# Optimization experiments

Hardware: AMD Instinct MI355X
Metric: run time of the kernel (lower is better)

The kernel has to match this reference:

```python
import jax, jax.numpy as jnp
import numpy as np

INPUT_SIZE = 1024
HIDDEN_SIZE = 1024

def _xavier(key, shape):
    fan_in, fan_out = shape
    limit = np.sqrt(6.0 / (fan_in + fan_out))
    return jax.random.uniform(key, shape, jnp.float32, -limit, limit)

def setup_inputs() -> dict:
    key = jax.random.key(0)
    ks = jax.random.split(key, 9)
    x = jax.random.normal(ks[0], (64, 512, INPUT_SIZE), jnp.float32)
    d = {"x": x}
    names_i = ["W_ii", "W_fi", "W_gi", "W_oi"]
    names_h = ["W_ih", "W_fh", "W_gh", "W_oh"]
    for n, k in zip(names_i, ks[1:5]):
        d[n] = _xavier(k, (INPUT_SIZE, HIDDEN_SIZE))
    for n, k in zip(names_h, ks[5:9]):
        d[n] = _xavier(k, (HIDDEN_SIZE, HIDDEN_SIZE))
    for n in ["b_ii", "b_ih", "b_fi", "b_fh", "b_gi", "b_gh", "b_oi", "b_oh"]:
        d[n] = jnp.zeros((HIDDEN_SIZE,), jnp.float32)
    return d

def _lstm(x, W_ii, W_ih, b_ii, b_ih, W_fi, W_fh, b_fi, b_fh,
          W_gi, W_gh, b_gi, b_gh, W_oi, W_oh, b_oi, b_oh):
    B, S, _ = x.shape
    H = W_ih.shape[0]
    # Fuse the 4 input-side GEMMs into one and hoist out of the recurrence.
    Wi = jnp.concatenate([W_ii, W_fi, W_gi, W_oi], axis=1)          # [I, 4H]
    Wh = jnp.concatenate([W_ih, W_fh, W_gh, W_oh], axis=1)          # [H, 4H]
    bi = jnp.concatenate([b_ii + b_ih, b_fi + b_fh, b_gi + b_gh, b_oi + b_oh])
    xproj = jnp.einsum('bsi,ig->bsg', x, Wi) + bi                    # [B, S, 4H]

    def step(carry, xp_t):
        h, c = carry
        gates = xp_t + h @ Wh                                        # [B, 4H]
        i_t = jax.nn.sigmoid(gates[:, 0 * H:1 * H])
        f_t = jax.nn.sigmoid(gates[:, 1 * H:2 * H])
        g_t = jnp.tanh(gates[:, 2 * H:3 * H])
        o_t = jax.nn.sigmoid(gates[:, 3 * H:4 * H])
        c = f_t * c + i_t * g_t
        h = o_t * jnp.tanh(c)
        return (h, c), None

    h0 = jnp.zeros((B, H), x.dtype)
    c0 = jnp.zeros((B, H), x.dtype)
    (h_t, c_t), _ = jax.lax.scan(step, (h0, c0), jnp.swapaxes(xproj, 0, 1))
    return h_t, c_t

def reference(x, W_ii, W_ih, b_ii, b_ih, W_fi, W_fh, b_fi, b_fh,
              W_gi, W_gh, b_gi, b_gh, W_oi, W_oh, b_oi, b_oh):
    return _lstm(x, W_ii, W_ih, b_ii, b_ih, W_fi, W_fh, b_fi, b_fh,
                 W_gi, W_gh, b_gi, b_gh, W_oi, W_oh, b_oi, b_oh)
```

## Files before the change

### kernel.cpp

```cpp
#include <hip/hip_runtime.h>
#include <hip/hip_bf16.h>

#define SEQ   512
#define HID   1024
#define NBLK  256
#define NTHR  256
#define PADK  2056
#define GPS   36
#define RSLOT 65792

typedef __attribute__((ext_vector_type(8))) short bf16x8;
typedef __attribute__((ext_vector_type(4))) float f32x4;
typedef __attribute__((ext_vector_type(2))) float f32x2;

struct Params {
  const float* x;
  const float* Wi[4];
  const float* Wh[4];
  const float* bi[4];
  const float* bh[4];
  float* out;
  const short* xbf;
  short* hring;
  short* hb0;
  short* hb1;
  unsigned* arrive;
  unsigned* gen;
};

__device__ __forceinline__ float sig_(float v)  { return 1.0f / (1.0f + __expf(-v)); }
__device__ __forceinline__ float tanh_(float v) { return 1.0f - 2.0f / (__expf(2.0f * v) + 1.0f); }

__device__ __forceinline__ short f2b(float f) {
  unsigned u = __builtin_bit_cast(unsigned, f);
  u += 0x7FFFu + ((u >> 16) & 1u);
  return (short)(u >> 16);
}
__device__ __forceinline__ bf16x8 cvt8(const float* p) {
  f32x4 a = *(const f32x4*)p;
  f32x4 b = *(const f32x4*)(p + 4);
  bf16x8 r;
  r[0] = f2b(a[0]); r[1] = f2b(a[1]); r[2] = f2b(a[2]); r[3] = f2b(a[3]);
  r[4] = f2b(b[0]); r[5] = f2b(b[1]); r[6] = f2b(b[2]); r[7] = f2b(b[3]);
  return r;
}

__device__ __forceinline__ bf16x8 ld16_sc1(const short* p) {
  bf16x8 r;
  asm volatile("global_load_dwordx4 %0, %1, off sc1" : "=v"(r) : "v"(p));
  return r;
}
__device__ __forceinline__ bf16x8 ld16_l2(const short* p) {
  bf16x8 r;
  asm volatile("global_load_dwordx4 %0, %1, off" : "=v"(r) : "v"(p));
  return r;
}
__device__ __forceinline__ void wait_vm0() {
  asm volatile("s_waitcnt vmcnt(0)" ::: "memory");
}

__global__ __launch_bounds__(256) void init_ws(unsigned* bar, unsigned* hzero, int hn) {
  int i = blockIdx.x * blockDim.x + threadIdx.x;
  if (i < 8448) bar[i] = 0u;
  if (i < hn) hzero[i] = 0u;
}

__global__ __launch_bounds__(256) void cvt_x(const float* __restrict__ x,
                                             short* __restrict__ xb) {
  size_t i = ((size_t)blockIdx.x * 256 + threadIdx.x) * 8;
  *(bf16x8*)(xb + i) = cvt8(x + i);
}

__device__ __forceinline__ void gbar_fence(unsigned* arrive, unsigned* gen,
                                           int tid, int bid, unsigned tgt) {
  __syncthreads();
  if (bid == 0) {
    if (tid != 0) {
      int polls = 0;
      while (__hip_atomic_load(&arrive[tid * 32], __ATOMIC_RELAXED,
                               __HIP_MEMORY_SCOPE_AGENT) < tgt) {
        __builtin_amdgcn_s_sleep(1);
        if (++polls > (1 << 22)) break;
      }
    }
    __syncthreads();
    if (tid == 0) {
      __threadfence();
      __hip_atomic_store(gen, tgt, __ATOMIC_RELEASE, __HIP_MEMORY_SCOPE_AGENT);
    }
    __syncthreads();
  } else {
    if (tid == 0) {
      __threadfence();
      __hip_atomic_store(&arrive[bid * 32], tgt, __ATOMIC_RELEASE,
                         __HIP_MEMORY_SCOPE_AGENT);
      int polls = 0;
      while (__hip_atomic_load(gen, __ATOMIC_RELAXED,
                               __HIP_MEMORY_SCOPE_AGENT) < tgt) {
        __builtin_amdgcn_s_sleep(1);
        if (++polls > (1 << 22)) break;
      }
      __threadfence();
    }
    __syncthreads();
  }
}

template <int MODE>
__global__ __launch_bounds__(NTHR, 1) void lstm_persistent(Params p) {
  extern __shared__ char smem[];
  short* bls    = (short*)smem;
  float* gparts = (float*)(smem + 131584);
  float* cst    = (float*)(smem + 131584 + 18432);
  float* bias_s = (float*)(smem + 131584 + 18432 + 1024);

  const int tid = threadIdx.x;
  const int bid = blockIdx.x;
  const int cg  = bid & 127;
  const int mh  = bid >> 7;
  const int r0  = mh * 32;
  const int j0  = cg * 8;

  {
    const int g    = tid & 3;
    const int krow = tid >> 2;
    const float* wi = p.Wi[g];
    const float* wh = p.Wh[g];
    for (int kb = 0; kb < 2048; kb += 64) {
      int k = kb + krow;
      const float* src = (k < HID) ? (wi + (size_t)k * HID + j0)
                                   : (wh + (size_t)(k - HID) * HID + j0);
      f32x4 va = *(const f32x4*)src;
      f32x4 vb = *(const f32x4*)(src + 4);
      #pragma unroll
      for (int jj = 0; jj < 4; ++jj) {
        bls[(4 * jj + g) * PADK + k]       = f2b(va[jj]);
        bls[(4 * (jj + 4) + g) * PADK + k] = f2b(vb[jj]);
      }
    }
  }
  if (tid < 32) {
    int g = tid & 3, j = j0 + (tid >> 2);
    bias_s[tid] = p.bi[g][j] + p.bh[g][j];
  }
  if (tid < 128) { cst[2 * tid] = 0.0f; cst[2 * tid + 1] = 0.0f; }
  __syncthreads();

  const int lane = tid & 63;
  const int ksl  = tid >> 6;
  const int m16  = lane & 15;
  const int quad = lane >> 4;
  const size_t rm0 = (size_t)(r0 + m16);
  const size_t rm1 = (size_t)(r0 + 16 + m16);
  const short* bB0 = bls + (size_t)m16 * PADK + ksl * 512 + quad * 8;
  const short* bB1 = bls + (size_t)(16 + m16) * PADK + ksl * 512 + quad * 8;

  const unsigned* myflag =
      p.arrive + (size_t)(mh * 128 + (ksl - 2) * 64 + lane);

  float cfin0 = 0.0f, cfin1 = 0.0f;

  for (int t = 0; t < SEQ; ++t) {
    f32x4 acc00 = {0,0,0,0}, acc01 = {0,0,0,0};
    f32x4 acc10 = {0,0,0,0}, acc11 = {0,0,0,0};

    if constexpr (MODE >= 1) {
      if (ksl < 2) {
        const short* xb = p.xbf + ksl * 512 + quad * 8 + (size_t)t * HID;
        const short* pa0 = xb + rm0 * (SEQ * HID);
        const short* pa1 = xb + rm1 * (SEQ * HID);
        #pragma unroll 4
        for (int ki = 0; ki < 16; ++ki) {
          bf16x8 a0 = *(const bf16x8*)(pa0 + ki * 32);
          bf16x8 a1 = *(const bf16x8*)(pa1 + ki * 32);
          bf16x8 b0 = *(const bf16x8*)(bB0 + ki * 32);
          bf16x8 b1 = *(const bf16x8*)(bB1 + ki * 32);
          acc00 = __builtin_amdgcn_mfma_f32_16x16x32_bf16(a0, b0, acc00, 0, 0, 0);
          acc01 = __builtin_amdgcn_mfma_f32_16x16x32_bf16(a0, b1, acc01, 0, 0, 0);
          acc10 = __builtin_amdgcn_mfma_f32_16x16x32_bf16(a1, b0, acc10, 0, 0, 0);
          acc11 = __builtin_amdgcn_mfma_f32_16x16x32_bf16(a1, b1, acc11, 0, 0, 0);
        }
      } else {
        if (t > 0) {
          int polls = 0;
          while (__hip_atomic_load(myflag, __ATOMIC_RELAXED,
                                   __HIP_MEMORY_SCOPE_AGENT) < (unsigned)t) {
            __builtin_amdgcn_s_sleep(1);
            if (++polls > (1 << 22)) break;
          }
        }
        const short* hr;
        if constexpr (MODE == 2)
          hr = p.hring + (size_t)t * RSLOT + (ksl - 2) * 512 + quad * 8;
        else
          hr = ((t & 1) ? p.hb1 : p.hb0) + (ksl - 2) * 512 + quad * 8;
        const short* pa0 = hr + rm0 * HID;
        const short* pa1 = hr + rm1 * HID;
        bf16x8 A0[16], A1[16];
        #pragma unroll
        for (int ki = 0; ki < 16; ++ki) {
          if constexpr (MODE == 2) {
            A0[ki] = ld16_l2(pa0 + ki * 32);
            A1[ki] = ld16_l2(pa1 + ki * 32);
          } else {
            A0[ki] = ld16_sc1(pa0 + ki * 32);
            A1[ki] = ld16_sc1(pa1 + ki * 32);
          }
        }
        wait_vm0();
        #pragma unroll
        for (int ki = 0; ki < 16; ++ki) {
          asm volatile("" : "+v"(A0[ki]));
          asm volatile("" : "+v"(A1[ki]));
        }
        #pragma unroll
        for (int ki = 0; ki < 16; ++ki) {
          bf16x8 b0 = *(const bf16x8*)(bB0 + ki * 32);
          bf16x8 b1 = *(const bf16x8*)(bB1 + ki * 32);
          acc00 = __builtin_amdgcn_mfma_f32_16x16x32_bf16(A0[ki], b0, acc00, 0, 0, 0);
          acc01 = __builtin_amdgcn_mfma_f32_16x16x32_bf16(A0[ki], b1, acc01, 0, 0, 0);
          acc10 = __builtin_amdgcn_mfma_f32_16x16x32_bf16(A1[ki], b0, acc10, 0, 0, 0);
          acc11 = __builtin_amdgcn_mfma_f32_16x16x32_bf16(A1[ki], b1, acc11, 0, 0, 0);
        }
      }
    } else {
      const float *fa0, *fa1;
      if (ksl < 2) {
        const float* xb = p.x + ksl * 512 + quad * 8 + (size_t)t * HID;
        fa0 = xb + rm0 * (SEQ * HID);
        fa1 = xb + rm1 * (SEQ * HID);
      } else {
        const float* hr = (p.out + ((t & 1) ? 65536 : 0)) + (ksl - 2) * 512 + quad * 8;
        fa0 = hr + rm0 * HID;
        fa1 = hr + rm1 * HID;
      }
      #pragma unroll 2
      for (int ki = 0; ki < 16; ++ki) {
        bf16x8 a0 = cvt8(fa0 + ki * 32);
        bf16x8 a1 = cvt8(fa1 + ki * 32);
        bf16x8 b0 = *(const bf16x8*)(bB0 + ki * 32);
        bf16x8 b1 = *(const bf16x8*)(bB1 + ki * 32);
        acc00 = __builtin_amdgcn_mfma_f32_16x16x32_bf16(a0, b0, acc00, 0, 0, 0);
        acc01 = __builtin_amdgcn_mfma_f32_16x16x32_bf16(a0, b1, acc01, 0, 0, 0);
        acc10 = __builtin_amdgcn_mfma_f32_16x16x32_bf16(a1, b0, acc10, 0, 0, 0);
        acc11 = __builtin_amdgcn_mfma_f32_16x16x32_bf16(a1, b1, acc11, 0, 0, 0);
      }
    }

    {
      float* gp = gparts + ksl * (32 * GPS);
      #pragma unroll
      for (int r = 0; r < 4; ++r) {
        gp[(quad * 4 + r) * GPS + m16]           = acc00[r];
        gp[(quad * 4 + r) * GPS + 16 + m16]      = acc01[r];
        gp[(16 + quad * 4 + r) * GPS + m16]      = acc10[r];
        gp[(16 + quad * 4 + r) * GPS + 16 + m16] = acc11[r];
      }
    }
    __syncthreads();

    if (tid < 128) {
      int rl = tid >> 2, jp = tid & 3;
      f32x4 ga = {0,0,0,0}, gb = {0,0,0,0};
      #pragma unroll
      for (int s = 0; s < 4; ++s) {
        const float* gp = gparts + s * (32 * GPS) + rl * GPS + jp * 8;
        ga += *(const f32x4*)gp;
        gb += *(const f32x4*)(gp + 4);
      }
      f32x4 ba = *(const f32x4*)(bias_s + jp * 8);
      f32x4 bb = *(const f32x4*)(bias_s + jp * 8 + 4);

      float i0 = sig_(ga[0] + ba[0]);
      float f0 = sig_(ga[1] + ba[1]);
      float g0 = tanh_(ga[2] + ba[2]);
      float o0 = sig_(ga[3] + ba[3]);
      float i1 = sig_(gb[0] + bb[0]);
      float f1 = sig_(gb[1] + bb[1]);
      float g1 = tanh_(gb[2] + bb[2]);
      float o1 = sig_(gb[3] + bb[3]);

      int ci = rl * 8 + jp * 2;
      float c0 = f0 * cst[ci]     + i0 * g0;
      float c1 = f1 * cst[ci + 1] + i1 * g1;
      cst[ci] = c0; cst[ci + 1] = c1;
      float h0v = o0 * tanh_(c0);
      float h1v = o1 * tanh_(c1);

      size_t off = (size_t)(r0 + rl) * HID + j0 + jp * 2;
      if constexpr (MODE >= 1) {
        unsigned u = (unsigned)(unsigned short)f2b(h0v) |
                     ((unsigned)(unsigned short)f2b(h1v) << 16);
        if (t < SEQ - 1) {
          short* hw;
          if constexpr (MODE == 2)
            hw = p.hring + (size_t)(t + 1) * RSLOT;
          else
            hw = (t & 1) ? p.hb0 : p.hb1;
          __hip_atomic_store((unsigned*)(hw + off), u, __ATOMIC_RELAXED,
                             __HIP_MEMORY_SCOPE_AGENT);
        } else {
          f32x2 hv = {h0v, h1v}; *(f32x2*)(p.out + off) = hv;
          f32x2 cv = {c0, c1};   *(f32x2*)(p.out + 65536 + off) = cv;
        }
      } else {
        float* hw = p.out + ((t & 1) ? 0 : 65536);
        f32x2 hv = {h0v, h1v};
        *(f32x2*)(hw + off) = hv;
        if (t == SEQ - 1) { cfin0 = c0; cfin1 = c1; }
      }
    }

    if constexpr (MODE >= 1) {
      __syncthreads();
      if (t < SEQ - 1 && tid == 0)
        __hip_atomic_store(&p.arrive[bid], (unsigned)(t + 1),
                           __ATOMIC_RELAXED, __HIP_MEMORY_SCOPE_AGENT);
    } else {
      if (t < SEQ - 1)
        gbar_fence(p.arrive, p.gen, tid, bid, (unsigned)(t + 1));
    }
  }

  if constexpr (MODE == 0) {
    if (tid < 128) {
      int rl = tid >> 2, jp = tid & 3;
      size_t off = (size_t)(r0 + rl) * HID + j0 + jp * 2;
      f32x2 cv = {cfin0, cfin1};
      *(f32x2*)(p.out + 65536 + off) = cv;
    }
  }
}

extern "C" void kernel_launch(void* const* d_in, const int* in_sizes, int n_in,
                              void* d_out, int out_size, void* d_ws, size_t ws_size,
                              hipStream_t stream) {
  Params prm;
  prm.x = (const float*)d_in[0];
  for (int g = 0; g < 4; ++g) {
    prm.Wi[g] = (const float*)d_in[1 + g];
    prm.Wh[g] = (const float*)d_in[5 + g];
    prm.bi[g] = (const float*)d_in[9 + 2 * g];
    prm.bh[g] = (const float*)d_in[10 + 2 * g];
  }
  prm.out    = (float*)d_out;
  prm.arrive = (unsigned*)d_ws;
  prm.gen    = prm.arrive + 8192;
  prm.xbf = nullptr; prm.hring = nullptr; prm.hb0 = nullptr; prm.hb1 = nullptr;

  const size_t XBF   = 67108864;
  const size_t need_pp   = 65536 + XBF + 2 * 131072;
  const size_t need_ring = 65536 + XBF + (size_t)SEQ * RSLOT * 2;
  int mode = 0;
  if (ws_size >= need_ring)      mode = 2;
  else if (ws_size >= need_pp)   mode = 1;

  if (mode >= 1) prm.xbf = (const short*)((char*)d_ws + 65536);
  if (mode == 2) {
    prm.hring = (short*)((char*)d_ws + 65536 + XBF);
  } else if (mode == 1) {
    prm.hb0 = (short*)((char*)d_ws + 65536 + XBF);
    prm.hb1 = prm.hb0 + 65536;
  }

  const int smem_bytes = 131584 + 18432 + 1024 + 128;
  hipFuncSetAttribute((const void*)lstm_persistent<2>,
                      hipFuncAttributeMaxDynamicSharedMemorySize, smem_bytes);
  hipFuncSetAttribute((const void*)lstm_persistent<1>,
                      hipFuncAttributeMaxDynamicSharedMemorySize, smem_bytes);
  hipFuncSetAttribute((const void*)lstm_persistent<0>,
                      hipFuncAttributeMaxDynamicSharedMemorySize, smem_bytes);

  if (mode == 2) {
    init_ws<<<256, 256, 0, stream>>>((unsigned*)d_ws, (unsigned*)prm.hring, 32768);
    cvt_x<<<16384, 256, 0, stream>>>(prm.x, (short*)prm.xbf);
    lstm_persistent<2><<<NBLK, NTHR, smem_bytes, stream>>>(prm);
  } else if (mode == 1) {
    init_ws<<<256, 256, 0, stream>>>((unsigned*)d_ws, (unsigned*)prm.hb0, 32768);
    cvt_x<<<16384, 256, 0, stream>>>(prm.x, (short*)prm.xbf);
    lstm_persistent<1><<<NBLK, NTHR, smem_bytes, stream>>>(prm);
  } else {
    init_ws<<<256, 256, 0, stream>>>((unsigned*)d_ws, (unsigned*)d_out, 65536);
    lstm_persistent<0><<<NBLK, NTHR, smem_bytes, stream>>>(prm);
  }
}
```

Baseline: 4.149 ms.

## Pad arrival flags, remap blocks, and skip zero h-slot in ring mode

New measurement: 3.730 ms. 10.1% less time.

```diff
diff --git a/kernel.cpp b/kernel.cpp
--- a/kernel.cpp
+++ b/kernel.cpp
@@ -7,7 +7,7 @@
 #define NTHR  256
 #define PADK  2056
 #define GPS   36
-#define RSLOT 65792
+#define HSLOT 65536
 
 typedef __attribute__((ext_vector_type(8))) short bf16x8;
 typedef __attribute__((ext_vector_type(4))) float f32x4;
@@ -116,8 +116,18 @@
 
   const int tid = threadIdx.x;
   const int bid = blockIdx.x;
-  const int cg  = bid & 127;
-  const int mh  = bid >> 7;
+
+  if constexpr (MODE == 2) __builtin_amdgcn_fence(__ATOMIC_ACQUIRE, "agent");
+
+  int cg, mh;
+  if constexpr (MODE == 2) {
+    mh = (bid >> 2) & 1;
+    cg = ((bid >> 3) << 2) | (bid & 3);
+  } else {
+    cg = bid & 127;
+    mh = bid >> 7;
+  }
+  const int lb  = mh * 128 + cg;
   const int r0  = mh * 32;
   const int j0  = cg * 8;
 
@@ -156,7 +166,7 @@
   const short* bB1 = bls + (size_t)(16 + m16) * PADK + ksl * 512 + quad * 8;
 
   const unsigned* myflag =
-      p.arrive + (size_t)(mh * 128 + (ksl - 2) * 64 + lane);
+      p.arrive + (size_t)(mh * 128 + (ksl - 2) * 64 + lane) * 32;
 
   float cfin0 = 0.0f, cfin1 = 0.0f;
 
@@ -180,8 +190,8 @@
           acc10 = __builtin_amdgcn_mfma_f32_16x16x32_bf16(a1, b0, acc10, 0, 0, 0);
           acc11 = __builtin_amdgcn_mfma_f32_16x16x32_bf16(a1, b1, acc11, 0, 0, 0);
         }
-      } else {
-        if (t > 0) {
+      } else if (t > 0) {
+        {
           int polls = 0;
           while (__hip_atomic_load(myflag, __ATOMIC_RELAXED,
                                    __HIP_MEMORY_SCOPE_AGENT) < (unsigned)t) {
@@ -191,7 +201,7 @@
         }
         const short* hr;
         if constexpr (MODE == 2)
-          hr = p.hring + (size_t)t * RSLOT + (ksl - 2) * 512 + quad * 8;
+          hr = p.hring + (size_t)(t - 1) * HSLOT + (ksl - 2) * 512 + quad * 8;
         else
           hr = ((t & 1) ? p.hb1 : p.hb0) + (ksl - 2) * 512 + quad * 8;
         const short* pa0 = hr + rm0 * HID;
@@ -294,7 +304,7 @@
         if (t < SEQ - 1) {
           short* hw;
           if constexpr (MODE == 2)
-            hw = p.hring + (size_t)(t + 1) * RSLOT;
+            hw = p.hring + (size_t)t * HSLOT;
           else
             hw = (t & 1) ? p.hb0 : p.hb1;
           __hip_atomic_store((unsigned*)(hw + off), u, __ATOMIC_RELAXED,
@@ -314,7 +324,7 @@
     if constexpr (MODE >= 1) {
       __syncthreads();
       if (t < SEQ - 1 && tid == 0)
-        __hip_atomic_store(&p.arrive[bid], (unsigned)(t + 1),
+        __hip_atomic_store(&p.arrive[(size_t)lb * 32], (unsigned)(t + 1),
                            __ATOMIC_RELAXED, __HIP_MEMORY_SCOPE_AGENT);
     } else {
       if (t < SEQ - 1)
@@ -349,11 +359,11 @@
   prm.xbf = nullptr; prm.hring = nullptr; prm.hb0 = nullptr; prm.hb1 = nullptr;
 
   const size_t XBF   = 67108864;
-  const size_t need_pp   = 65536 + XBF + 2 * 131072;
-  const size_t need_ring = 65536 + XBF + (size_t)SEQ * RSLOT * 2;
+  const size_t need1 = 65536 + XBF + 2 * 131072;
+  const size_t need2 = 65536 + XBF + (size_t)(SEQ - 1) * 131072;
   int mode = 0;
-  if (ws_size >= need_ring)      mode = 2;
-  else if (ws_size >= need_pp)   mode = 1;
+  if (ws_size >= need2)      mode = 2;
+  else if (ws_size >= need1) mode = 1;
 
   if (mode >= 1) prm.xbf = (const short*)((char*)d_ws + 65536);
   if (mode == 2) {
@@ -372,7 +382,7 @@
                       hipFuncAttributeMaxDynamicSharedMemorySize, smem_bytes);
 
   if (mode == 2) {
-    init_ws<<<256, 256, 0, stream>>>((unsigned*)d_ws, (unsigned*)prm.hring, 32768);
+    init_ws<<<256, 256, 0, stream>>>((unsigned*)d_ws, (unsigned*)d_ws, 0);
     cvt_x<<<16384, 256, 0, stream>>>(prm.x, (short*)prm.xbf);
     lstm_persistent<2><<<NBLK, NTHR, smem_bytes, stream>>>(prm);
   } else if (mode == 1) {
```
